# Optimization experiments

Hardware: AMD Instinct MI355X
Metric: run time of the kernel (lower is better)

Reference implementation:

```python
import jax, jax.numpy as jnp
import numpy as np

EMB = 768
HEADS = 12
DH = EMB // HEADS


def setup_inputs() -> dict:
    key = jax.random.key(0)
    k = jax.random.split(key, 5)
    s = 0.02
    return {
        "x": jax.random.normal(k[0], (4, 2048, EMB), dtype=jnp.float32),
        "qkv_w": jax.random.normal(k[1], (3 * EMB, EMB), dtype=jnp.float32) * s,  # torch Linear weight [out,in]
        "qkv_b": jax.random.normal(k[2], (3 * EMB,), dtype=jnp.float32) * s,
        "proj_w": jax.random.normal(k[3], (EMB, EMB), dtype=jnp.float32) * s,
        "proj_b": jax.random.normal(k[4], (EMB,), dtype=jnp.float32) * s,
    }


def reference(x, qkv_w, qkv_b, proj_w, proj_b):
    b, n, _ = x.shape
    qkv = x @ qkv_w.T + qkv_b  # [b, n, 3*EMB]
    # rearrange 'b n (h d qkv) -> qkv b h n d'
    qkv = qkv.reshape(b, n, HEADS, DH, 3)
    qkv = jnp.transpose(qkv, (4, 0, 2, 1, 3))  # [3, b, h, n, d]
    q, k, v = qkv[0], qkv[1], qkv[2]
    e = jnp.einsum("bhqd,bhkd->bhqk", q, k)
    scale = jnp.float32(EMB) ** 0.5
    # NOTE: original divides by sqrt(emb_size) AFTER softmax (faithful to source)
    attn = jax.nn.softmax(e, axis=-1) / scale
    out = jnp.einsum("bhqk,bhkd->bhqd", attn, v)
    out = jnp.transpose(out, (0, 2, 1, 3)).reshape(b, n, EMB)  # 'b h n d -> b n (h d)'
    return out @ proj_w.T + proj_b
```

## Files before the change

### kernel.cpp

```cpp
#include <hip/hip_runtime.h>
#include <hip/hip_bf16.h>

typedef unsigned short ushort_t;
typedef __attribute__((ext_vector_type(8))) short s16x8;
typedef __attribute__((ext_vector_type(4))) float f32x4;
typedef __attribute__((ext_vector_type(16))) float f32x16;
typedef __attribute__((ext_vector_type(4))) unsigned int u32x4;

#define EMB 768
#define HEADS 12
#define DH 64
#define BATCH 4
#define SEQ 2048
#define MTOK (BATCH*SEQ)
#define NQKV (3*EMB)
#define NBH (BATCH*HEADS)
#define LOG2E 1.44269504088896f

__device__ __forceinline__ ushort_t f2bf(float f) {
  unsigned u = __float_as_uint(f);
  u += 0x7fffu + ((u >> 16) & 1u);
  return (ushort_t)(u >> 16);
}
__device__ __forceinline__ unsigned pk2bf(float a, float b) {
  return (unsigned)f2bf(a) | ((unsigned)f2bf(b) << 16);
}
__device__ __forceinline__ unsigned cvtpk(float lo, float hi_) {
  unsigned d;
  asm("v_cvt_pk_bf16_f32 %0, %1, %2" : "=v"(d) : "v"(lo), "v"(hi_));
  return d;
}

__device__ __forceinline__ void gload_lds16(const void* g, void* l) {
  __builtin_amdgcn_global_load_lds(
      (const __attribute__((address_space(1))) unsigned*)g,
      (__attribute__((address_space(3))) unsigned*)l, 16, 0, 0);
}

__global__ void cvt_bf16(const float* __restrict__ in, ushort_t* __restrict__ out, int n4) {
  int i = blockIdx.x * blockDim.x + threadIdx.x;
  if (i >= n4) return;
  const float4 v = reinterpret_cast<const float4*>(in)[i];
  reinterpret_cast<uint2*>(out)[i] = make_uint2(pk2bf(v.x, v.y), pk2bf(v.z, v.w));
}

__global__ void cvt_wqkv(const float* __restrict__ w, const float* __restrict__ bias,
                         ushort_t* __restrict__ out, float* __restrict__ bias_p, int n4) {
  int i = blockIdx.x * blockDim.x + threadIdx.x;
  if (i >= n4) return;
  const int srcrow = i / 192;
  const int c4 = i - srcrow * 192;
  const int h = srcrow / 192;
  const int rem = srcrow - h * 192;
  const int d = rem / 3;
  const int which = rem - d * 3;
  const int dstrow = which * 768 + h * 64 + d;
  const float4 v = reinterpret_cast<const float4*>(w)[i];
  reinterpret_cast<uint2*>(out)[dstrow * 192 + c4] =
      make_uint2(pk2bf(v.x, v.y), pk2bf(v.z, v.w));
  if (c4 == 0) bias_p[dstrow] = bias[srcrow];
}

#define TM 128
#define TN 128
#define BKG 64
#define GSTEPS 12

template<int MODE>
__global__ __launch_bounds__(256, 2) void gemm_bt(
    const ushort_t* __restrict__ A, const ushort_t* __restrict__ BT,
    const float* __restrict__ bias, float* __restrict__ Cf,
    ushort_t* __restrict__ Qd, ushort_t* __restrict__ Kd, ushort_t* __restrict__ Vt,
    int M, int N, int K)
{
  __shared__ alignas(16) ushort_t As[2][TM*BKG];
  __shared__ alignas(16) ushort_t Bs[2][TN*BKG];
  const int t = threadIdx.x;
  const int w = t >> 6, l = t & 63, g = l >> 4, r = l & 15;
  const int wr = w >> 1, wc = w & 1;
  int lin = blockIdx.y * gridDim.x + blockIdx.x;
  const int cpx = (gridDim.x * gridDim.y) >> 3;
  lin = (lin & 7) * cpx + (lin >> 3);
  const int m0 = (lin / gridDim.x) * TM, n0 = (lin - (lin / gridDim.x) * gridDim.x) * TN;

  f32x4 acc[4][4] = {};

#define GSTAGE(bufc, st)                                                           \
  {                                                                                \
    const int kt = (st) * BKG;                                                     \
    _Pragma("unroll")                                                              \
    for (int p = 0; p < 4; ++p) {                                                  \
      const int off = (t + p*256) * 16;                     \
      const int row = off >> 7;                                  \
      const int scb = (off & 127) ^ ((row & 7) << 4);                              \
      gload_lds16(A  + (size_t)(m0+row)*K + kt + (scb>>1), (char*)&As[bufc][0] + off); \
      gload_lds16(BT + (size_t)(n0+row)*K + kt + (scb>>1), (char*)&Bs[bufc][0] + off); \
    }                                                                              \
  }

#define GCOMP(bufc)                                                                \
  {                                                                                \
    s16x8 fa[4][2], fb[4][2];                                                      \
    _Pragma("unroll")                                                              \
    for (int mi = 0; mi < 4; ++mi)                                                 \
      _Pragma("unroll")                                                            \
      for (int kk = 0; kk < 2; ++kk) {                                             \
        const int ra = wr*64 + mi*16 + r;                                          \
        fa[mi][kk] = *(const s16x8*)((const char*)&As[bufc][0] + ra*128 +          \
                                     ((g*16 + kk*64) ^ ((ra&7)<<4)));              \
        const int rb = wc*64 + mi*16 + r;                                          \
        fb[mi][kk] = *(const s16x8*)((const char*)&Bs[bufc][0] + rb*128 +          \
                                     ((g*16 + kk*64) ^ ((rb&7)<<4)));              \
      }                                                                            \
    __builtin_amdgcn_s_setprio(1);                                                 \
    _Pragma("unroll")                                                              \
    for (int mi = 0; mi < 4; ++mi)                                                 \
      _Pragma("unroll")                                                            \
      for (int ni = 0; ni < 4; ++ni) {                                             \
        acc[mi][ni] = __builtin_amdgcn_mfma_f32_16x16x32_bf16(                     \
            fa[mi][0], fb[ni][0], acc[mi][ni], 0, 0, 0);                           \
        acc[mi][ni] = __builtin_amdgcn_mfma_f32_16x16x32_bf16(                     \
            fa[mi][1], fb[ni][1], acc[mi][ni], 0, 0, 0);                           \
      }                                                                            \
    __builtin_amdgcn_s_setprio(0);                                                 \
  }

#define GITER(cur, st)                                                             \
  {                                                                                \
    asm volatile("s_barrier" ::: "memory");                                        \
    { const int s1 = (st) + 1 < GSTEPS ? (st) + 1 : GSTEPS - 1;                    \
      GSTAGE((cur) ^ 1, s1); }                                                     \
    asm volatile("s_waitcnt vmcnt(8)" ::: "memory");                               \
    asm volatile("s_barrier" ::: "memory");                                        \
    GCOMP(cur);                                                                    \
  }

  GSTAGE(0, 0);
#pragma unroll
  for (int s = 0; s < GSTEPS; ++s) GITER(s & 1, s);
#undef GITER
#undef GCOMP
#undef GSTAGE

#pragma unroll
  for (int ni = 0; ni < 4; ++ni) {
    const int col = n0 + wc*64 + ni*16 + r;
    const float bv = bias[col];
    if (MODE == 0) {
#pragma unroll
      for (int mi = 0; mi < 4; ++mi)
#pragma unroll
        for (int q = 0; q < 4; ++q) {
          const int rowg = m0 + wr*64 + mi*16 + g*4 + q;
          Cf[(size_t)rowg * N + col] = acc[mi][ni][q] + bv;
        }
    } else {
      const int which = col / 768;
      const int h_ = (col - which * 768) >> 6;
      const int d_ = col & 63;
      if (which == 2) {
#pragma unroll
        for (int mi = 0; mi < 4; ++mi) {
          const int nn0 = m0 + wr*64 + mi*16 + g*4;
          const int bb = nn0 >> 11, nl = nn0 & 2047;
          const int np0 = (nl & ~12) | ((nl & 4) << 1) | ((nl & 8) >> 1);
          uint2 u;
          u.x = pk2bf(acc[mi][ni][0] + bv, acc[mi][ni][1] + bv);
          u.y = pk2bf(acc[mi][ni][2] + bv, acc[mi][ni][3] + bv);
          *reinterpret_cast<uint2*>(Vt + ((size_t)(bb*HEADS + h_)*DH + d_)*SEQ + np0) = u;
        }
      } else {
        ushort_t* dst = (which == 0) ? Qd : Kd;
        const float sc = (which == 0) ? LOG2E : 1.0f;
#pragma unroll
        for (int mi = 0; mi < 4; ++mi)
#pragma unroll
          for (int q = 0; q < 4; ++q) {
            const int rowg = m0 + wr*64 + mi*16 + g*4 + q;
            const int bb = rowg >> 11, nn = rowg & 2047;
            dst[((size_t)(bb*HEADS + h_)*SEQ + nn)*DH + d_] =
                f2bf((acc[mi][ni][q] + bv) * sc);
          }
      }
    }
  }
}

#define NTILH 16

__global__ __launch_bounds__(256, 3) void attn_fwd(
    const ushort_t* __restrict__ Qd, const ushort_t* __restrict__ Kd,
    const ushort_t* __restrict__ Vt, ushort_t* __restrict__ Op0,
    ushort_t* __restrict__ Op1, float* __restrict__ Lp)
{
  __shared__ alignas(16) char L[2][16384];
  char* Lc = &L[0][0];

  const int t = threadIdx.x;
  const int w = t >> 6, l = t & 63;
  const int c31 = l & 31, hi = l >> 5;
  const int blk = blockIdx.x;
  const int logical = (blk & 7) * 192 + (blk >> 3);
  const int bh = logical >> 5;
  const int rem = logical & 31;
  const int half = rem >> 4;
  const int qt = rem & 15;
  const int q0 = qt * 128 + w * 32;
  const int tb = half * NTILH;

  const ushort_t* Qp = Qd + (size_t)bh * SEQ * DH;
  const ushort_t* Kp = Kd + (size_t)bh * SEQ * DH;
  const ushort_t* Vp = Vt + (size_t)bh * DH * SEQ;

  s16x8 qf[4];
  {
    const ushort_t* qp = Qp + (size_t)(q0 + c31) * DH + hi * 8;
#pragma unroll
    for (int c = 0; c < 4; ++c) qf[c] = *(const s16x8*)(qp + c * 16);
  }

  f32x16 oacc0 = {}, oacc1 = {};
  float ps0 = 0.f, ps1 = 0.f, ps2 = 0.f, ps3 = 0.f;

  const int ldsb = hi * 1024 + c31 * 16;
  const ushort_t* ksrc0 = Kp + (size_t)l * DH + w * 16;
  const ushort_t* vsrc0 = Vp + (size_t)l * SEQ + w * 16;
  char* kdst0 = Lc + w * 2048 + l * 16;

#define STAGE(bufc, tile_)                                                         \
  {                                                                                \
    const int tl = (tile_);                                                        \
    const ushort_t* ks = ksrc0 + (size_t)tl * (64 * DH);                           \
    const ushort_t* vs = vsrc0 + tl * 64;                                          \
    char* kd = kdst0 + (bufc) * 16384;                                             \
    gload_lds16(ks,     kd);                                                       \
    gload_lds16(ks + 8, kd + 1024);                                                \
    gload_lds16(vs,     kd + 8192);                                                \
    gload_lds16(vs + 8, kd + 9216);                                                \
  }

#define KGROUP(bufc, kg)                                                           \
  {                                                                                \
    const char* base = Lc + (bufc) * 16384 + ldsb;                                 \
    s16x8 kf0 = *(const s16x8*)(base + ((kg)*512 + 0*2048));                       \
    s16x8 kf1 = *(const s16x8*)(base + ((kg)*512 + 1*2048));                       \
    s16x8 kf2 = *(const s16x8*)(base + ((kg)*512 + 2*2048));                       \
    s16x8 kf3 = *(const s16x8*)(base + ((kg)*512 + 3*2048));                       \
    s16x8 va00 = *(const s16x8*)(base + (8192 + (kg)*4096 + 0*2048 + 0*512));      \
    s16x8 va01 = *(const s16x8*)(base + (8192 + (kg)*4096 + 1*2048 + 0*512));      \
    s16x8 va10 = *(const s16x8*)(base + (8192 + (kg)*4096 + 0*2048 + 1*512));      \
    s16x8 va11 = *(const s16x8*)(base + (8192 + (kg)*4096 + 1*2048 + 1*512));      \
    __builtin_amdgcn_s_setprio(1);                                                 \
    f32x16 s = {};                                                                 \
    s = __builtin_amdgcn_mfma_f32_32x32x16_bf16(kf0, qf[0], s, 0, 0, 0);           \
    s = __builtin_amdgcn_mfma_f32_32x32x16_bf16(kf1, qf[1], s, 0, 0, 0);           \
    s = __builtin_amdgcn_mfma_f32_32x32x16_bf16(kf2, qf[2], s, 0, 0, 0);           \
    s = __builtin_amdgcn_mfma_f32_32x32x16_bf16(kf3, qf[3], s, 0, 0, 0);           \
    __builtin_amdgcn_s_setprio(0);                                                 \
    float pe[16];                                                                  \
    _Pragma("unroll")                                                              \
    for (int r2 = 0; r2 < 16; ++r2) pe[r2] = __builtin_amdgcn_exp2f(s[r2]);        \
    ps0 += (pe[0]  + pe[1])  + (pe[2]  + pe[3]);                                   \
    ps1 += (pe[4]  + pe[5])  + (pe[6]  + pe[7]);                                   \
    ps2 += (pe[8]  + pe[9])  + (pe[10] + pe[11]);                                  \
    ps3 += (pe[12] + pe[13]) + (pe[14] + pe[15]);                                  \
    u32x4 f0u = { cvtpk(pe[0],  pe[1]),  cvtpk(pe[2],  pe[3]),                     \
                  cvtpk(pe[4],  pe[5]),  cvtpk(pe[6],  pe[7]) };                   \
    u32x4 f1u = { cvtpk(pe[8],  pe[9]),  cvtpk(pe[10], pe[11]),                    \
                  cvtpk(pe[12], pe[13]), cvtpk(pe[14], pe[15]) };                  \
    const s16x8 pf0 = __builtin_bit_cast(s16x8, f0u);                              \
    const s16x8 pf1 = __builtin_bit_cast(s16x8, f1u);                              \
    __builtin_amdgcn_s_setprio(1);                                                 \
    oacc0 = __builtin_amdgcn_mfma_f32_32x32x16_bf16(va00, pf0, oacc0, 0, 0, 0);    \
    oacc0 = __builtin_amdgcn_mfma_f32_32x32x16_bf16(va01, pf1, oacc0, 0, 0, 0);    \
    oacc1 = __builtin_amdgcn_mfma_f32_32x32x16_bf16(va10, pf0, oacc1, 0, 0, 0);    \
    oacc1 = __builtin_amdgcn_mfma_f32_32x32x16_bf16(va11, pf1, oacc1, 0, 0, 0);    \
    __builtin_amdgcn_s_setprio(0);                                                 \
  }

#define ITER(cur, tt)                                                              \
  {                                                                                \
    asm volatile("s_barrier" ::: "memory");                                        \
    { const int n1 = (tt) + 1 < NTILH ? (tt) + 1 : NTILH - 1;                      \
      STAGE((cur) ^ 1, tb + n1); }                                                 \
    asm volatile("s_waitcnt vmcnt(4)" ::: "memory");                               \
    asm volatile("s_barrier" ::: "memory");                                        \
    KGROUP(cur, 0);                                                                \
    KGROUP(cur, 1);                                                                \
  }

  STAGE(0, tb);
  for (int tt = 0; tt < NTILH; tt += 2) {
    ITER(0, tt);
    ITER(1, tt + 1);
  }
#undef ITER
#undef KGROUP
#undef STAGE

  const float psum = (ps0 + ps1) + (ps2 + ps3);
  const float lt = psum + __shfl_xor(psum, 32);

  ushort_t* Op = half ? Op1 : Op0;
  ushort_t* op = Op + ((size_t)bh * SEQ + q0 + c31) * DH;
#pragma unroll
  for (int f = 0; f < 2; ++f) {
    const f32x16& o = f ? oacc1 : oacc0;
#pragma unroll
    for (int rq = 0; rq < 4; ++rq) {
      const int dbase = f * 32 + 8 * rq + 4 * hi;
      uint2 u;
      u.x = pk2bf(o[rq*4+0], o[rq*4+1]);
      u.y = pk2bf(o[rq*4+2], o[rq*4+3]);
      *reinterpret_cast<uint2*>(op + dbase) = u;
    }
  }
  if (l < 32)
    Lp[(size_t)half * (NBH * SEQ) + (size_t)bh * SEQ + q0 + c31] = lt;
}

__global__ void attn_combine(const ushort_t* __restrict__ Op0,
                             const ushort_t* __restrict__ Op1,
                             const float* __restrict__ Lp,
                             ushort_t* __restrict__ Oa) {
  const int i = blockIdx.x * blockDim.x + threadIdx.x;
  const int dseg = (i & 7) * 8;
  const int n = (i >> 3) & (SEQ - 1);
  const int bh = i >> 14;
  const int b = bh / HEADS, h = bh - b * HEADS;
  const size_t src = ((size_t)bh * SEQ + n) * DH + dseg;
  const u32x4 a = *reinterpret_cast<const u32x4*>(Op0 + src);
  const u32x4 c = *reinterpret_cast<const u32x4*>(Op1 + src);
  const float lsum = Lp[(size_t)bh * SEQ + n] + Lp[(size_t)NBH * SEQ + (size_t)bh * SEQ + n];
  const float s = 0.036084391824351615f / lsum;
  u32x4 rr;
#pragma unroll
  for (int j = 0; j < 4; ++j) {
    const unsigned x = a[j], y = c[j];
    const float x0 = __uint_as_float(x << 16), x1 = __uint_as_float(x & 0xffff0000u);
    const float y0 = __uint_as_float(y << 16), y1 = __uint_as_float(y & 0xffff0000u);
    rr[j] = pk2bf((x0 + y0) * s, (x1 + y1) * s);
  }
  *reinterpret_cast<u32x4*>(Oa + ((size_t)(b * SEQ + n) * EMB + h * DH + dseg)) = rr;
}

extern "C" void kernel_launch(void* const* d_in, const int* in_sizes, int n_in,
                              void* d_out, int out_size, void* d_ws, size_t ws_size,
                              hipStream_t stream) {
  const float* x      = (const float*)d_in[0];
  const float* qkv_w  = (const float*)d_in[1];
  const float* qkv_b  = (const float*)d_in[2];
  const float* proj_w = (const float*)d_in[3];
  const float* proj_b = (const float*)d_in[4];
  float* out = (float*)d_out;

  ushort_t* xb    = (ushort_t*)d_ws;
  ushort_t* wqkv  = xb    + (size_t)MTOK*EMB;
  ushort_t* wproj = wqkv  + (size_t)NQKV*EMB;
  ushort_t* Qd    = wproj + (size_t)EMB*EMB;
  ushort_t* Kd    = Qd    + (size_t)MTOK*EMB;
  ushort_t* Vt    = Kd    + (size_t)MTOK*EMB;
  ushort_t* Oa    = Vt    + (size_t)MTOK*EMB;
  float*    biasp = (float*)(Oa + (size_t)MTOK*EMB);
  ushort_t* Op1   = (ushort_t*)(biasp + 4096);
  float*    Lp    = (float*)(Op1 + (size_t)MTOK*EMB);
  ushort_t* Op0   = xb;

  {
    int n4 = MTOK*EMB/4;
    cvt_bf16<<<(n4+255)/256, 256, 0, stream>>>(x, xb, n4);
  }
  {
    int n4 = NQKV*EMB/4;
    cvt_wqkv<<<(n4+255)/256, 256, 0, stream>>>(qkv_w, qkv_b, wqkv, biasp, n4);
  }
  {
    int n4 = EMB*EMB/4;
    cvt_bf16<<<(n4+255)/256, 256, 0, stream>>>(proj_w, wproj, n4);
  }

  gemm_bt<1><<<dim3(NQKV/TN, MTOK/TM), 256, 0, stream>>>(
      xb, wqkv, biasp, nullptr, Qd, Kd, Vt, MTOK, NQKV, EMB);

  attn_fwd<<<1536, 256, 0, stream>>>(Qd, Kd, Vt, Op0, Op1, Lp);

  attn_combine<<<(NBH*SEQ*8)/256, 256, 0, stream>>>(Op0, Op1, Lp, Oa);

  gemm_bt<0><<<dim3(EMB/TN, MTOK/TM), 256, 0, stream>>>(
      Oa, wproj, proj_b, out, nullptr, nullptr, nullptr, MTOK, EMB, EMB);
}
```

Measured before the change: 153.9 us.

## Double query rows per wave and triple-buffer K/V tiles in attention

Each wave now handles 64 query rows (two 32-row MFMA tiles) instead of 32, so every K/V fragment read from LDS feeds twice as many MFMAs, and the grid is halved to 768 blocks. The K/V staging moves from a double buffer to a triple buffer with a prefetch distance of two tiles and a matching vmcnt wait. The aim is to reduce LDS traffic and global loads per unit of work and to hide more load latency. In exchange, register pressure roughly doubles for accumulators and Q fragments, which may lower occupancy under launch_bounds(256,3), and LDS use per block grows to 48KB.

After: 208.0 us. 35.1% more time.

```diff
diff --git a/kernel.cpp b/kernel.cpp
--- a/kernel.cpp
+++ b/kernel.cpp
@@ -193,34 +193,37 @@
     const ushort_t* __restrict__ Vt, ushort_t* __restrict__ Op0,
     ushort_t* __restrict__ Op1, float* __restrict__ Lp)
 {
-  __shared__ alignas(16) char L[2][16384];
+  __shared__ alignas(16) char L[3][16384];
   char* Lc = &L[0][0];
 
   const int t = threadIdx.x;
   const int w = t >> 6, l = t & 63;
   const int c31 = l & 31, hi = l >> 5;
   const int blk = blockIdx.x;
-  const int logical = (blk & 7) * 192 + (blk >> 3);
-  const int bh = logical >> 5;
-  const int rem = logical & 31;
-  const int half = rem >> 4;
-  const int qt = rem & 15;
-  const int q0 = qt * 128 + w * 32;
+  const int logical = (blk & 7) * 96 + (blk >> 3);
+  const int bh = logical >> 4;
+  const int rem = logical & 15;
+  const int half = rem >> 3;
+  const int qt = rem & 7;
+  const int q0 = qt * 256 + w * 64;
   const int tb = half * NTILH;
 
   const ushort_t* Qp = Qd + (size_t)bh * SEQ * DH;
   const ushort_t* Kp = Kd + (size_t)bh * SEQ * DH;
   const ushort_t* Vp = Vt + (size_t)bh * DH * SEQ;
 
-  s16x8 qf[4];
+  s16x8 qf0[4], qf1[4];
   {
-    const ushort_t* qp = Qp + (size_t)(q0 + c31) * DH + hi * 8;
-#pragma unroll
-    for (int c = 0; c < 4; ++c) qf[c] = *(const s16x8*)(qp + c * 16);
-  }
-
-  f32x16 oacc0 = {}, oacc1 = {};
-  float ps0 = 0.f, ps1 = 0.f, ps2 = 0.f, ps3 = 0.f;
+    const ushort_t* qp0 = Qp + (size_t)(q0 + c31) * DH + hi * 8;
+    const ushort_t* qp1 = qp0 + 32 * DH;
+#pragma unroll
+    for (int c = 0; c < 4; ++c) { qf0[c] = *(const s16x8*)(qp0 + c*16);
+                                  qf1[c] = *(const s16x8*)(qp1 + c*16); }
+  }
+
+  f32x16 oa00 = {}, oa01 = {};
+  f32x16 oa10 = {}, oa11 = {};
+  float ps00 = 0.f, ps01 = 0.f, ps10 = 0.f, ps11 = 0.f;
 
   const int ldsb = hi * 1024 + c31 * 16;
   const ushort_t* ksrc0 = Kp + (size_t)l * DH + w * 16;
@@ -251,72 +254,99 @@
     s16x8 va10 = *(const s16x8*)(base + (8192 + (kg)*4096 + 0*2048 + 1*512));      \
     s16x8 va11 = *(const s16x8*)(base + (8192 + (kg)*4096 + 1*2048 + 1*512));      \
     __builtin_amdgcn_s_setprio(1);                                                 \
-    f32x16 s = {};                                                                 \
-    s = __builtin_amdgcn_mfma_f32_32x32x16_bf16(kf0, qf[0], s, 0, 0, 0);           \
-    s = __builtin_amdgcn_mfma_f32_32x32x16_bf16(kf1, qf[1], s, 0, 0, 0);           \
-    s = __builtin_amdgcn_mfma_f32_32x32x16_bf16(kf2, qf[2], s, 0, 0, 0);           \
-    s = __builtin_amdgcn_mfma_f32_32x32x16_bf16(kf3, qf[3], s, 0, 0, 0);           \
+    f32x16 s0 = {}, s1 = {};                                                       \
+    s0 = __builtin_amdgcn_mfma_f32_32x32x16_bf16(kf0, qf0[0], s0, 0, 0, 0);        \
+    s1 = __builtin_amdgcn_mfma_f32_32x32x16_bf16(kf0, qf1[0], s1, 0, 0, 0);        \
+    s0 = __builtin_amdgcn_mfma_f32_32x32x16_bf16(kf1, qf0[1], s0, 0, 0, 0);        \
+    s1 = __builtin_amdgcn_mfma_f32_32x32x16_bf16(kf1, qf1[1], s1, 0, 0, 0);        \
+    s0 = __builtin_amdgcn_mfma_f32_32x32x16_bf16(kf2, qf0[2], s0, 0, 0, 0);        \
+    s1 = __builtin_amdgcn_mfma_f32_32x32x16_bf16(kf2, qf1[2], s1, 0, 0, 0);        \
+    s0 = __builtin_amdgcn_mfma_f32_32x32x16_bf16(kf3, qf0[3], s0, 0, 0, 0);        \
+    s1 = __builtin_amdgcn_mfma_f32_32x32x16_bf16(kf3, qf1[3], s1, 0, 0, 0);        \
     __builtin_amdgcn_s_setprio(0);                                                 \
-    float pe[16];                                                                  \
+    float pe0[16], pe1[16];                                                        \
     _Pragma("unroll")                                                              \
-    for (int r2 = 0; r2 < 16; ++r2) pe[r2] = __builtin_amdgcn_exp2f(s[r2]);        \
-    ps0 += (pe[0]  + pe[1])  + (pe[2]  + pe[3]);                                   \
-    ps1 += (pe[4]  + pe[5])  + (pe[6]  + pe[7]);                                   \
-    ps2 += (pe[8]  + pe[9])  + (pe[10] + pe[11]);                                  \
-    ps3 += (pe[12] + pe[13]) + (pe[14] + pe[15]);                                  \
-    u32x4 f0u = { cvtpk(pe[0],  pe[1]),  cvtpk(pe[2],  pe[3]),                     \
-                  cvtpk(pe[4],  pe[5]),  cvtpk(pe[6],  pe[7]) };                   \
-    u32x4 f1u = { cvtpk(pe[8],  pe[9]),  cvtpk(pe[10], pe[11]),                    \
-                  cvtpk(pe[12], pe[13]), cvtpk(pe[14], pe[15]) };                  \
-    const s16x8 pf0 = __builtin_bit_cast(s16x8, f0u);                              \
-    const s16x8 pf1 = __builtin_bit_cast(s16x8, f1u);                              \
+    for (int r2 = 0; r2 < 16; ++r2) {                                              \
+      pe0[r2] = __builtin_amdgcn_exp2f(s0[r2]);                                    \
+      pe1[r2] = __builtin_amdgcn_exp2f(s1[r2]);                                    \
+    }                                                                              \
+    ps00 += ((pe0[0]+pe0[1])+(pe0[2]+pe0[3])) + ((pe0[4]+pe0[5])+(pe0[6]+pe0[7])); \
+    ps01 += ((pe0[8]+pe0[9])+(pe0[10]+pe0[11]))+((pe0[12]+pe0[13])+(pe0[14]+pe0[15]));\
+    ps10 += ((pe1[0]+pe1[1])+(pe1[2]+pe1[3])) + ((pe1[4]+pe1[5])+(pe1[6]+pe1[7])); \
+    ps11 += ((pe1[8]+pe1[9])+(pe1[10]+pe1[11]))+((pe1[12]+pe1[13])+(pe1[14]+pe1[15]));\
+    u32x4 a0 = { cvtpk(pe0[0],  pe0[1]),  cvtpk(pe0[2],  pe0[3]),                  \
+                 cvtpk(pe0[4],  pe0[5]),  cvtpk(pe0[6],  pe0[7]) };                \
+    u32x4 a1 = { cvtpk(pe0[8],  pe0[9]),  cvtpk(pe0[10], pe0[11]),                 \
+                 cvtpk(pe0[12], pe0[13]), cvtpk(pe0[14], pe0[15]) };               \
+    u32x4 b0 = { cvtpk(pe1[0],  pe1[1]),  cvtpk(pe1[2],  pe1[3]),                  \
+                 cvtpk(pe1[4],  pe1[5]),  cvtpk(pe1[6],  pe1[7]) };                \
+    u32x4 b1 = { cvtpk(pe1[8],  pe1[9]),  cvtpk(pe1[10], pe1[11]),                 \
+                 cvtpk(pe1[12], pe1[13]), cvtpk(pe1[14], pe1[15]) };               \
+    const s16x8 pf00 = __builtin_bit_cast(s16x8, a0);                              \
+    const s16x8 pf01 = __builtin_bit_cast(s16x8, a1);                              \
+    const s16x8 pf10 = __builtin_bit_cast(s16x8, b0);                              \
+    const s16x8 pf11 = __builtin_bit_cast(s16x8, b1);                              \
     __builtin_amdgcn_s_setprio(1);                                                 \
-    oacc0 = __builtin_amdgcn_mfma_f32_32x32x16_bf16(va00, pf0, oacc0, 0, 0, 0);    \
-    oacc0 = __builtin_amdgcn_mfma_f32_32x32x16_bf16(va01, pf1, oacc0, 0, 0, 0);    \
-    oacc1 = __builtin_amdgcn_mfma_f32_32x32x16_bf16(va10, pf0, oacc1, 0, 0, 0);    \
-    oacc1 = __builtin_amdgcn_mfma_f32_32x32x16_bf16(va11, pf1, oacc1, 0, 0, 0);    \
+    oa00 = __builtin_amdgcn_mfma_f32_32x32x16_bf16(va00, pf00, oa00, 0, 0, 0);     \
+    oa00 = __builtin_amdgcn_mfma_f32_32x32x16_bf16(va01, pf01, oa00, 0, 0, 0);     \
+    oa01 = __builtin_amdgcn_mfma_f32_32x32x16_bf16(va10, pf00, oa01, 0, 0, 0);     \
+    oa01 = __builtin_amdgcn_mfma_f32_32x32x16_bf16(va11, pf01, oa01, 0, 0, 0);     \
+    oa10 = __builtin_amdgcn_mfma_f32_32x32x16_bf16(va00, pf10, oa10, 0, 0, 0);     \
+    oa10 = __builtin_amdgcn_mfma_f32_32x32x16_bf16(va01, pf11, oa10, 0, 0, 0);     \
+    oa11 = __builtin_amdgcn_mfma_f32_32x32x16_bf16(va10, pf10, oa11, 0, 0, 0);     \
+    oa11 = __builtin_amdgcn_mfma_f32_32x32x16_bf16(va11, pf11, oa11, 0, 0, 0);     \
     __builtin_amdgcn_s_setprio(0);                                                 \
   }
 
-#define ITER(cur, tt)                                                              \
+#define ITER(bufcur, bufn2, tt)                                                    \
   {                                                                                \
     asm volatile("s_barrier" ::: "memory");                                        \
-    { const int n1 = (tt) + 1 < NTILH ? (tt) + 1 : NTILH - 1;                      \
-      STAGE((cur) ^ 1, tb + n1); }                                                 \
-    asm volatile("s_waitcnt vmcnt(4)" ::: "memory");                               \
+    const int nt2 = (tt) + 2 < NTILH ? (tt) + 2 : NTILH - 1;                       \
+    STAGE(bufn2, tb + nt2);                                                        \
+    asm volatile("s_waitcnt vmcnt(8)" ::: "memory");                               \
     asm volatile("s_barrier" ::: "memory");                                        \
-    KGROUP(cur, 0);                                                                \
-    KGROUP(cur, 1);                                                                \
+    KGROUP(bufcur, 0);                                                             \
+    KGROUP(bufcur, 1);                                                             \
   }
 
   STAGE(0, tb);
-  for (int tt = 0; tt < NTILH; tt += 2) {
-    ITER(0, tt);
-    ITER(1, tt + 1);
-  }
+  STAGE(1, tb + 1);
+  for (int tt = 0; tt < NTILH - 1; tt += 3) {
+    ITER(0, 2, tt);
+    ITER(1, 0, tt + 1);
+    ITER(2, 1, tt + 2);
+  }
+  ITER(0, 2, 15);
 #undef ITER
 #undef KGROUP
 #undef STAGE
 
-  const float psum = (ps0 + ps1) + (ps2 + ps3);
-  const float lt = psum + __shfl_xor(psum, 32);
+  const float psum0 = ps00 + ps01;
+  const float psum1 = ps10 + ps11;
+  const float lt0 = psum0 + __shfl_xor(psum0, 32);
+  const float lt1 = psum1 + __shfl_xor(psum1, 32);
 
   ushort_t* Op = half ? Op1 : Op0;
-  ushort_t* op = Op + ((size_t)bh * SEQ + q0 + c31) * DH;
-#pragma unroll
-  for (int f = 0; f < 2; ++f) {
-    const f32x16& o = f ? oacc1 : oacc0;
-#pragma unroll
-    for (int rq = 0; rq < 4; ++rq) {
-      const int dbase = f * 32 + 8 * rq + 4 * hi;
-      uint2 u;
-      u.x = pk2bf(o[rq*4+0], o[rq*4+1]);
-      u.y = pk2bf(o[rq*4+2], o[rq*4+3]);
-      *reinterpret_cast<uint2*>(op + dbase) = u;
+#pragma unroll
+  for (int j = 0; j < 2; ++j) {
+    ushort_t* op = Op + ((size_t)bh * SEQ + q0 + j*32 + c31) * DH;
+#pragma unroll
+    for (int f = 0; f < 2; ++f) {
+      const f32x16& o = j ? (f ? oa11 : oa10) : (f ? oa01 : oa00);
+#pragma unroll
+      for (int rq = 0; rq < 4; ++rq) {
+        const int dbase = f * 32 + 8 * rq + 4 * hi;
+        uint2 u;
+        u.x = pk2bf(o[rq*4+0], o[rq*4+1]);
+        u.y = pk2bf(o[rq*4+2], o[rq*4+3]);
+        *reinterpret_cast<uint2*>(op + dbase) = u;
+      }
     }
   }
-  if (l < 32)
-    Lp[(size_t)half * (NBH * SEQ) + (size_t)bh * SEQ + q0 + c31] = lt;
+  if (l < 32) {
+    Lp[(size_t)half * (NBH * SEQ) + (size_t)bh * SEQ + q0 + c31] = lt0;
+    Lp[(size_t)half * (NBH * SEQ) + (size_t)bh * SEQ + q0 + 32 + c31] = lt1;
+  }
 }
 
 __global__ void attn_combine(const ushort_t* __restrict__ Op0,
@@ -382,7 +412,7 @@
   gemm_bt<1><<<dim3(NQKV/TN, MTOK/TM), 256, 0, stream>>>(
       xb, wqkv, biasp, nullptr, Qd, Kd, Vt, MTOK, NQKV, EMB);
 
-  attn_fwd<<<1536, 256, 0, stream>>>(Qd, Kd, Vt, Op0, Op1, Lp);
+  attn_fwd<<<768, 256, 0, stream>>>(Qd, Kd, Vt, Op0, Op1, Lp);
 
   attn_combine<<<(NBH*SEQ*8)/256, 256, 0, stream>>>(Op0, Op1, Lp, Oa);
 
```
